# Kernel tuning notes

Measured on AMD Instinct MI355X. Metric: run time of the kernel, lower is better.

The kernel has to match this reference:

```python
import jax, jax.numpy as jnp
import numpy as np

N_NODES = 100000
N_EDGES = 1600000


def setup_inputs() -> dict:
    key = jax.random.key(0)
    k1, k2, k3, k4, k5, k6 = jax.random.split(key, 6)
    x = jax.random.normal(k1, (N_NODES, 2), dtype=jnp.float32)
    edge_index = jax.random.randint(k2, (2, N_EDGES), 0, N_NODES, dtype=jnp.int64)
    # Glorot-style init for GCN weights, zeros for biases (PyG defaults)
    W1 = jax.random.normal(k3, (2, 64), dtype=jnp.float32) * (1.0 / np.sqrt(2.0))
    b1 = jnp.zeros((64,), dtype=jnp.float32)
    W2 = jax.random.normal(k4, (64, 1), dtype=jnp.float32) * (1.0 / np.sqrt(64.0))
    b2 = jnp.zeros((1,), dtype=jnp.float32)
    return {"x": x, "edge_index": edge_index, "W1": W1, "b1": b1, "W2": W2, "b2": b2}


def reference(x, edge_index, W1, b1, W2, b2):
    N = x.shape[0]
    row, col = edge_index[0], edge_index[1]  # source, target (PyG flow source_to_target)
    # symmetric GCN normalization, degrees from target index (no self loops)
    deg = jax.ops.segment_sum(jnp.ones(edge_index.shape[1], x.dtype), col, num_segments=N)
    deg_inv_sqrt = jnp.where(deg > 0, jnp.where(deg > 0, deg, 1.0) ** -0.5, 0.0)
    norm = (deg_inv_sqrt[row] * deg_inv_sqrt[col])[:, None]  # [E,1]

    def gcn_conv(h, W, b):
        h = h @ W                       # [N,F_out] tiny GEMM
        msg = h[row] * norm             # gather + scale: [E,F_out]
        agg = jax.ops.segment_sum(msg, col, num_segments=N)  # scatter-add
        return agg + b

    h = jax.nn.relu(gcn_conv(x, W1, b1))   # dropout is identity in eval mode
    out = jax.nn.relu(gcn_conv(h, W2, b2))
    return out
```

## Files before the change

### kernel.cpp

```cpp
#include <hip/hip_runtime.h>
#include <math.h>

#define NN 100000
#define NE 1600000
#define NB 391
#define EPB 4096
#define NPB 391
#define STRIDE 5120

__global__ void reorder_kernel(const int* __restrict__ row, const int* __restrict__ col,
                               int* __restrict__ cursor, unsigned* __restrict__ packed) {
    __shared__ int h[392], lb[392], gb[392];
    __shared__ int s[256];
    __shared__ unsigned st[EPB];
    __shared__ unsigned short sbkt[EPB];
    int t = threadIdx.x;
    int e0 = blockIdx.x * EPB;
    int n = min(EPB, NE - e0);

    for (int i = t; i < 392; i += 256) h[i] = 0;
    __syncthreads();

    unsigned pk[16]; int bb[16];
#pragma unroll
    for (int u = 0; u < 16; ++u) {
        int i = u * 256 + t;
        if (i < n) {
            int r = row[e0 + i], c = col[e0 + i];
            pk[u] = ((unsigned)r << 8) | (unsigned)(c & 255);
            bb[u] = c >> 8;
        } else bb[u] = -1;
    }
#pragma unroll
    for (int u = 0; u < 16; ++u)
        if (bb[u] >= 0) atomicAdd(&h[bb[u]], 1);
    __syncthreads();

    int a0 = h[2 * t], a1 = h[2 * t + 1];
    int pv = (t < 196) ? (a0 + a1) : 0;
    s[t] = pv;
    __syncthreads();
    for (int off = 1; off < 256; off <<= 1) {
        int u = (t >= off) ? s[t - off] : 0;
        __syncthreads();
        s[t] += u;
        __syncthreads();
    }
    int pex = s[t] - pv;
    lb[2 * t] = pex;
    lb[2 * t + 1] = pex + a0;
    for (int b = t; b < NB; b += 256) {
        int c = h[b];
        gb[b] = c ? atomicAdd(&cursor[b], c) : 0;
    }
    __syncthreads();
    for (int i = t; i < 392; i += 256) h[i] = 0;
    __syncthreads();

#pragma unroll
    for (int u = 0; u < 16; ++u) {
        if (bb[u] >= 0) {
            int r = atomicAdd(&h[bb[u]], 1);
            int idx = lb[bb[u]] + r;
            st[idx] = pk[u];
            sbkt[idx] = (unsigned short)bb[u];
        }
    }
    __syncthreads();
    for (int i = t; i < n; i += 256) {
        int b = sbkt[i];
        int pos = gb[b] + (i - lb[b]);
        if (pos < STRIDE)
            packed[b * STRIDE + pos] = st[i];
    }
}

__global__ void sortb_kernel(const unsigned* __restrict__ packed, const int* __restrict__ cursor,
                             const float2* __restrict__ x2,
                             unsigned* __restrict__ srow, int2* __restrict__ node_rng,
                             float* __restrict__ dis, float2* __restrict__ y2) {
    __shared__ int cnt[256], scn[256], rk[256], sexA[256];
    __shared__ unsigned st[STRIDE];
    __shared__ unsigned srt[STRIDE];
    int t = threadIdx.x;
    int b = blockIdx.x;
    int s0 = b * STRIDE;
    int L = min(cursor[b], STRIDE);

    cnt[t] = 0; rk[t] = 0;
    __syncthreads();
    for (int i = t; i < L; i += 256) {
        unsigned p = packed[s0 + i];
        st[i] = p;
        atomicAdd(&cnt[p & 255u], 1);
    }
    __syncthreads();
    int v = cnt[t];
    scn[t] = v;
    __syncthreads();
    for (int off = 1; off < 256; off <<= 1) {
        int u = (t >= off) ? scn[t - off] : 0;
        __syncthreads();
        scn[t] += u;
        __syncthreads();
    }
    int sex = scn[t] - v;
    sexA[t] = sex;
    __syncthreads();

    int node = (b << 8) + t;
    if (node < NN) {
        float dv = (v > 0) ? rsqrtf((float)v) : 0.0f;
        dis[node] = dv;
        float2 xv = x2[node];
        y2[node] = make_float2(xv.x * dv, xv.y * dv);
        node_rng[node] = make_int2(s0 + sex, s0 + sex + v);
    }

    for (int i = t; i < L; i += 256) {
        unsigned p = st[i];
        int cl = p & 255u;
        int r = atomicAdd(&rk[cl], 1);
        srt[sexA[cl] + r] = p >> 8;
    }
    __syncthreads();
    for (int i = t; i < L; i += 256) srow[s0 + i] = srt[i];
}

__global__ void conv1_kernel(const unsigned* __restrict__ srow, const int2* __restrict__ node_rng,
                             const float2* __restrict__ y2, const float* __restrict__ dis,
                             const float* __restrict__ W1, const float* __restrict__ b1,
                             const float* __restrict__ W2, float* __restrict__ z2) {
    __shared__ float sW0[64], sW1[64], sb1[64], sW2[64];
    int t = threadIdx.x;
    if (t < 64) { sW0[t] = W1[t]; sW1[t] = W1[64 + t]; sb1[t] = b1[t]; sW2[t] = W2[t]; }
    __syncthreads();
    int lane = t & 3;
    int node = blockIdx.x * 64 + (t >> 2);
    if (node >= NN) return;
    int2 rng = node_rng[node];
    float sx = 0.f, sy = 0.f;
    for (int k = rng.x + lane; k < rng.y; k += 4) {
        float2 v = y2[srow[k]];
        sx += v.x; sy += v.y;
    }
    sx += __shfl_xor(sx, 1); sy += __shfl_xor(sy, 1);
    sx += __shfl_xor(sx, 2); sy += __shfl_xor(sy, 2);
    float dv = dis[node];
    float a0 = sx * dv, a1 = sy * dv;
    float acc = 0.0f;
    int j0 = lane * 16;
#pragma unroll
    for (int jj = 0; jj < 16; ++jj) {
        int j = j0 + jj;
        float h = fmaf(a0, sW0[j], fmaf(a1, sW1[j], sb1[j]));
        acc = fmaf(fmaxf(h, 0.0f), sW2[j], acc);
    }
    acc += __shfl_xor(acc, 1);
    acc += __shfl_xor(acc, 2);
    if (lane == 0) z2[node] = acc * dv;
}

__global__ void conv2_kernel(const unsigned* __restrict__ srow, const int2* __restrict__ node_rng,
                             const float* __restrict__ z2, const float* __restrict__ dis,
                             const float* __restrict__ b2, float* __restrict__ out) {
    int t = threadIdx.x;
    int lane = t & 3;
    int node = blockIdx.x * 64 + (t >> 2);
    if (node >= NN) return;
    int2 rng = node_rng[node];
    float s = 0.f;
    for (int k = rng.x + lane; k < rng.y; k += 4)
        s += z2[srow[k]];
    s += __shfl_xor(s, 1);
    s += __shfl_xor(s, 2);
    if (lane == 0)
        out[node] = fmaxf(fmaf(dis[node], s, b2[0]), 0.0f);
}

extern "C" void kernel_launch(void* const* d_in, const int* in_sizes, int n_in,
                              void* d_out, int out_size, void* d_ws, size_t ws_size,
                              hipStream_t stream) {
    const float* x  = (const float*)d_in[0];
    const int*   ei = (const int*)d_in[1];
    const float* W1 = (const float*)d_in[2];
    const float* b1 = (const float*)d_in[3];
    const float* W2 = (const float*)d_in[4];
    const float* b2 = (const float*)d_in[5];
    float* out = (float*)d_out;

    const int* row = ei;
    const int* col = ei + NE;

    unsigned* packed   = (unsigned*)d_ws;
    unsigned* srow     = packed + (size_t)NB * STRIDE;
    float2*   y2       = (float2*)(srow + (size_t)NB * STRIDE);
    float*    dis      = (float*)(y2 + NN);
    float*    z2       = dis + NN;
    int2*     node_rng = (int2*)(z2 + NN);
    int*      cursor   = (int*)(node_rng + NN);

    hipMemsetAsync(cursor, 0, NB * sizeof(int), stream);

    reorder_kernel<<<NPB, 256, 0, stream>>>(row, col, cursor, packed);
    sortb_kernel  <<<NB, 256, 0, stream>>>(packed, cursor, (const float2*)x,
                                           srow, node_rng, dis, y2);
    conv1_kernel  <<<(NN + 63) / 64, 256, 0, stream>>>(srow, node_rng, y2, dis,
                                                       W1, b1, W2, z2);
    conv2_kernel  <<<(NN + 63) / 64, 256, 0, stream>>>(srow, node_rng, z2, dis, b2, out);
}
```

Before: 125.8 us.

## Halve node bucket width to 128 and scatter sorted rows directly to global

Buckets now cover 128 nodes instead of 256, which doubles the bucket count to 782 and halves the edges each reorder block handles to 2048. The scan and bookkeeping are reworked to four buckets per thread in reorder and 128 active threads in sortb. sortb drops its second shared staging buffer and writes each sorted row straight to its final global slot. The aim is more blocks to fill the GPU's compute units and less shared memory per block, at the cost of more global cursor atomics and less coalesced global writes.

```diff
diff --git a/kernel.cpp b/kernel.cpp
--- a/kernel.cpp
+++ b/kernel.cpp
@@ -3,14 +3,17 @@
 
 #define NN 100000
 #define NE 1600000
-#define NB 391
-#define EPB 4096
-#define NPB 391
-#define STRIDE 5120
+#define BSHIFT 7
+#define BKT 128
+#define NB 782
+#define NBP 784
+#define EPB 2048
+#define NPB 782
+#define STRIDE 2560
 
 __global__ void reorder_kernel(const int* __restrict__ row, const int* __restrict__ col,
                                int* __restrict__ cursor, unsigned* __restrict__ packed) {
-    __shared__ int h[392], lb[392], gb[392];
+    __shared__ int h[NBP], lb[NBP], gb[NBP];
     __shared__ int s[256];
     __shared__ unsigned st[EPB];
     __shared__ unsigned short sbkt[EPB];
@@ -18,26 +21,29 @@
     int e0 = blockIdx.x * EPB;
     int n = min(EPB, NE - e0);
 
-    for (int i = t; i < 392; i += 256) h[i] = 0;
-    __syncthreads();
-
-    unsigned pk[16]; int bb[16];
-#pragma unroll
-    for (int u = 0; u < 16; ++u) {
+    for (int i = t; i < NBP; i += 256) h[i] = 0;
+    __syncthreads();
+
+    unsigned pk[8]; int bb[8];
+#pragma unroll
+    for (int u = 0; u < 8; ++u) {
         int i = u * 256 + t;
         if (i < n) {
             int r = row[e0 + i], c = col[e0 + i];
-            pk[u] = ((unsigned)r << 8) | (unsigned)(c & 255);
-            bb[u] = c >> 8;
+            pk[u] = ((unsigned)r << BSHIFT) | (unsigned)(c & (BKT - 1));
+            bb[u] = c >> BSHIFT;
         } else bb[u] = -1;
     }
 #pragma unroll
-    for (int u = 0; u < 16; ++u)
+    for (int u = 0; u < 8; ++u)
         if (bb[u] >= 0) atomicAdd(&h[bb[u]], 1);
     __syncthreads();
 
-    int a0 = h[2 * t], a1 = h[2 * t + 1];
-    int pv = (t < 196) ? (a0 + a1) : 0;
+    int b0 = 0, b1 = 0, b2 = 0, b3 = 0, pv = 0;
+    if (t < 196) {
+        b0 = h[4 * t]; b1 = h[4 * t + 1]; b2 = h[4 * t + 2]; b3 = h[4 * t + 3];
+        pv = b0 + b1 + b2 + b3;
+    }
     s[t] = pv;
     __syncthreads();
     for (int off = 1; off < 256; off <<= 1) {
@@ -46,19 +52,23 @@
         s[t] += u;
         __syncthreads();
     }
-    int pex = s[t] - pv;
-    lb[2 * t] = pex;
-    lb[2 * t + 1] = pex + a0;
+    if (t < 196) {
+        int pex = s[t] - pv;
+        lb[4 * t] = pex;
+        lb[4 * t + 1] = pex + b0;
+        lb[4 * t + 2] = pex + b0 + b1;
+        lb[4 * t + 3] = pex + b0 + b1 + b2;
+    }
     for (int b = t; b < NB; b += 256) {
         int c = h[b];
         gb[b] = c ? atomicAdd(&cursor[b], c) : 0;
     }
     __syncthreads();
-    for (int i = t; i < 392; i += 256) h[i] = 0;
-    __syncthreads();
-
-#pragma unroll
-    for (int u = 0; u < 16; ++u) {
+    for (int i = t; i < NBP; i += 256) h[i] = 0;
+    __syncthreads();
+
+#pragma unroll
+    for (int u = 0; u < 8; ++u) {
         if (bb[u] >= 0) {
             int r = atomicAdd(&h[bb[u]], 1);
             int idx = lb[bb[u]] + r;
@@ -79,52 +89,49 @@
                              const float2* __restrict__ x2,
                              unsigned* __restrict__ srow, int2* __restrict__ node_rng,
                              float* __restrict__ dis, float2* __restrict__ y2) {
-    __shared__ int cnt[256], scn[256], rk[256], sexA[256];
+    __shared__ int cnt[BKT], scn[BKT], rk[BKT], sexA[BKT];
     __shared__ unsigned st[STRIDE];
-    __shared__ unsigned srt[STRIDE];
     int t = threadIdx.x;
     int b = blockIdx.x;
     int s0 = b * STRIDE;
     int L = min(cursor[b], STRIDE);
 
-    cnt[t] = 0; rk[t] = 0;
+    if (t < BKT) { cnt[t] = 0; rk[t] = 0; }
     __syncthreads();
     for (int i = t; i < L; i += 256) {
         unsigned p = packed[s0 + i];
         st[i] = p;
-        atomicAdd(&cnt[p & 255u], 1);
-    }
-    __syncthreads();
-    int v = cnt[t];
-    scn[t] = v;
-    __syncthreads();
-    for (int off = 1; off < 256; off <<= 1) {
-        int u = (t >= off) ? scn[t - off] : 0;
-        __syncthreads();
-        scn[t] += u;
-        __syncthreads();
-    }
-    int sex = scn[t] - v;
-    sexA[t] = sex;
-    __syncthreads();
-
-    int node = (b << 8) + t;
-    if (node < NN) {
-        float dv = (v > 0) ? rsqrtf((float)v) : 0.0f;
-        dis[node] = dv;
-        float2 xv = x2[node];
-        y2[node] = make_float2(xv.x * dv, xv.y * dv);
-        node_rng[node] = make_int2(s0 + sex, s0 + sex + v);
-    }
-
+        atomicAdd(&cnt[p & (BKT - 1u)], 1);
+    }
+    __syncthreads();
+    if (t < BKT) scn[t] = cnt[t];
+    __syncthreads();
+    for (int off = 1; off < BKT; off <<= 1) {
+        int u = (t < BKT && t >= off) ? scn[t - off] : 0;
+        __syncthreads();
+        if (t < BKT) scn[t] += u;
+        __syncthreads();
+    }
+    if (t < BKT) {
+        int v = cnt[t];
+        int sex = scn[t] - v;
+        sexA[t] = sex;
+        int node = (b << BSHIFT) + t;
+        if (node < NN) {
+            float dv = (v > 0) ? rsqrtf((float)v) : 0.0f;
+            dis[node] = dv;
+            float2 xv = x2[node];
+            y2[node] = make_float2(xv.x * dv, xv.y * dv);
+            node_rng[node] = make_int2(s0 + sex, s0 + sex + v);
+        }
+    }
+    __syncthreads();
     for (int i = t; i < L; i += 256) {
         unsigned p = st[i];
-        int cl = p & 255u;
+        int cl = p & (BKT - 1u);
         int r = atomicAdd(&rk[cl], 1);
-        srt[sexA[cl] + r] = p >> 8;
-    }
-    __syncthreads();
-    for (int i = t; i < L; i += 256) srow[s0 + i] = srt[i];
+        srow[s0 + sexA[cl] + r] = p >> BSHIFT;
+    }
 }
 
 __global__ void conv1_kernel(const unsigned* __restrict__ srow, const int2* __restrict__ node_rng,
```

After: 141.7 us. 1.13x slower.
